# Performance work log

Hardware: AMD Instinct MI355X
Metric: run time of the kernel (lower is better)

## Reference

```python
import jax, jax.numpy as jnp
import numpy as np

B, N, NFEAT = 8, 5000, 15
NUM_CLASSES_IN = 12          # len(elem_labels)
D_IN = NUM_CLASSES_IN + NFEAT - 1  # 26
D_DIST = 256
D_HID = 256
BIN_SIZE = 100
NBINS = N // BIN_SIZE        # 50
K = 16                       # num_neighbors
DIST_MULT = 0.1
MAX_HALF_BINS = 100          # max_num_bins // 2
NUM_ID_OUT, NUM_REG_OUT = 8, 4


def _pairwise_dist(A):
    # A: [nbins, bs, d] -> [nbins, bs, bs]
    na = jnp.sum(A * A, -1)
    d2 = na[..., :, None] - 2.0 * jnp.einsum('...nd,...md->...nm', A, A) + na[..., None, :]
    return jnp.sqrt(jnp.maximum(d2, 1e-6))


def _build_edges(points, rot):
    # points: [N, D_DIST]; LSH binning then per-bin kNN (exp(-dist_mult * dist) affinities)
    mul = points @ rot[:, :NBINS // 2]
    cmul = jnp.concatenate([mul, -mul], axis=-1)
    bin_idx = jnp.argmax(cmul, axis=-1)
    bins_split = jnp.argsort(bin_idx).reshape(NBINS, BIN_SIZE)   # [nbins, bs] point ids
    parts = points[bins_split]                                   # [nbins, bs, d]
    dm = jnp.exp(-DIST_MULT * _pairwise_dist(parts))             # [nbins, bs, bs]
    vals, idx = jax.lax.top_k(dm, K)                             # [nbins, bs, K]
    dst = jax.vmap(lambda b, i: b[i])(bins_split, idx)           # global dst ids
    src = jnp.broadcast_to(bins_split[:, :, None], dst.shape)
    return src.reshape(-1), dst.reshape(-1), vals.reshape(-1)    # nnz = N*K


def _ghconv(x, src, dst, vals, theta, W_h, W_t, b_t):
    # x: [N, H]; edge list (src, dst, vals); duplicates sum, matching tf.sparse.add
    deg = jax.ops.segment_sum(vals, src, num_segments=N)
    norm = jnp.power(deg + 1e-6, -0.5)[:, None]
    f_hom = (x @ theta) * norm
    agg = jax.ops.segment_sum(vals[:, None] * f_hom[dst], src, num_segments=N) * norm
    f_het = x @ W_h
    gate = jax.nn.sigmoid(x @ W_t + b_t)
    return jax.nn.selu(gate * agg + (1.0 - gate) * f_het)


def setup_inputs() -> dict:
    key = jax.random.key(0)
    ks = jax.random.split(key, 32)
    w = lambda i, shape, s=0.02: (s * jax.random.normal(ks[i], shape)).astype(jnp.float32)
    ids = jax.random.randint(ks[0], (B, N, 1), 0, NUM_CLASSES_IN).astype(jnp.float32)
    props = jax.random.normal(ks[1], (B, N, NFEAT - 1), dtype=jnp.float32)
    X = jnp.concatenate([ids, props], axis=-1)
    return {
        'X': X,
        'rot': w(2, (D_DIST, MAX_HALF_BINS), 1.0),
        'W_emb': w(3, (D_IN, D_DIST)), 'b_emb': w(4, (D_DIST,)),
        'Wenc_id': w(5, (D_IN, D_HID)), 'benc_id': w(6, (D_HID,)),
        'theta_id': w(7, (D_HID, D_HID)), 'Wh_id': w(8, (D_HID, D_HID)),
        'Wt_id': w(9, (D_HID, D_HID)), 'bt_id': w(10, (D_HID,)),
        'Wdec_id': w(11, (D_HID, D_HID)), 'bdec_id': w(12, (D_HID,)),
        'Wout_id': w(13, (D_HID, NUM_ID_OUT)), 'bout_id': w(14, (NUM_ID_OUT,)),
        'Wenc_reg': w(15, (D_IN, D_HID)), 'benc_reg': w(16, (D_HID,)),
        'theta_reg': w(17, (D_HID, D_HID)), 'Wh_reg': w(18, (D_HID, D_HID)),
        'Wt_reg': w(19, (D_HID, D_HID)), 'bt_reg': w(20, (D_HID,)),
        'Wdec_reg': w(21, (D_HID, D_HID)), 'bdec_reg': w(22, (D_HID,)),
        'Wout_reg': w(23, (D_HID, NUM_REG_OUT)), 'bout_reg': w(24, (NUM_REG_OUT,)),
    }


def reference(X, rot, W_emb, b_emb,
              Wenc_id, benc_id, theta_id, Wh_id, Wt_id, bt_id, Wdec_id, bdec_id, Wout_id, bout_id,
              Wenc_reg, benc_reg, theta_reg, Wh_reg, Wt_reg, bt_reg, Wdec_reg, bdec_reg, Wout_reg, bout_reg):
    # InputEncoding: one-hot class id + remaining features
    enc = jnp.concatenate(
        [jax.nn.one_hot(X[:, :, 0].astype(jnp.int32), NUM_CLASSES_IN, dtype=jnp.float32),
         X[:, :, 1:]], axis=-1)                                  # [B, N, 26]
    emb = enc @ W_emb + b_emb                                     # distance embedding
    src, dst, vals = jax.vmap(_build_edges, in_axes=(0, None))(emb, rot)

    def branch(Wenc, benc, theta, Wh, Wt, bt, Wdec, bdec, Wout, bout):
        x = jax.nn.selu(enc @ Wenc + benc)
        x = jax.vmap(lambda xb, s, d, v: _ghconv(xb, s, d, v, theta, Wh, Wt, bt))(x, src, dst, vals)
        x = jax.nn.selu(x @ Wdec + bdec)
        return x @ Wout + bout

    out_id = branch(Wenc_id, benc_id, theta_id, Wh_id, Wt_id, bt_id, Wdec_id, bdec_id, Wout_id, bout_id)
    out_reg = branch(Wenc_reg, benc_reg, theta_reg, Wh_reg, Wt_reg, bt_reg, Wdec_reg, bdec_reg, Wout_reg, bout_reg)
    return out_id, out_reg
```

## Files before the change

kernel.cpp:

```cpp
#include <hip/hip_runtime.h>
#include <hip/hip_bf16.h>
#include <cstdint>
#include <cstddef>

#define NB     8
#define NLOC   5000
#define NPTS   40000
#define DIN    26
#define DH     256
#define NBINS  50
#define BSZ    100
#define KNN    16
#define KP     104

static const size_t OFF_BHI  = 40960000;
static const size_t OFF_BLO  = 41353216;
static const size_t OFF_BDHI = 41746432;
static const size_t OFF_BDLO = 41877504;
static const size_t OFF_ENC  = 81920000;
static const size_t OFF_BIN  = 86080000;
static const size_t OFF_ORD  = 86240000;
static const size_t OFF_NRM  = 86400000;
static const size_t OFF_EVAL = 86560000;
static const size_t OFF_EDST = 89120000;
static const size_t OFF_KEYS = 91680000;
static const size_t OFF_AXHI = 91680000;
static const size_t OFF_AXLO = 112160000;
static const size_t OFF_NA   = 132640000;
static const size_t OFF_FHET = 132640000;
static const size_t OFF_GATE = 173600000;

typedef __attribute__((ext_vector_type(8))) short short8;
typedef __attribute__((ext_vector_type(4))) float f32x4;

__device__ __forceinline__ float selu_f(float x) {
  const float scale = 1.0507009873554805f, alpha = 1.6732632423543772f;
  return x > 0.f ? scale * x : scale * alpha * expm1f(x);
}

__device__ __forceinline__ void split_bf16(float v, __hip_bfloat16& h, __hip_bfloat16& l) {
  h = __float2bfloat16(v);
  l = __float2bfloat16(v - __bfloat162float(h));
}

#define EPB 16
__global__ __launch_bounds__(256) void k_enc_emb(
    const float* __restrict__ X, const float* __restrict__ Wemb,
    const float* __restrict__ bemb, float* __restrict__ enc,
    double* __restrict__ emb, double* __restrict__ na_u) {
  __shared__ float xb[EPB * 15];
  __shared__ double partd[EPB][4];
  const int tid = threadIdx.x;
  const int lane = tid & 63, wid = tid >> 6;
  const int r0 = blockIdx.x * EPB;
  if (tid < EPB * 15) xb[tid] = X[(size_t)r0 * 15 + tid];
  double wcol[DIN];
  #pragma unroll
  for (int c = 0; c < DIN; c++) wcol[c] = (double)Wemb[c * DH + tid];
  const double bcol = (double)bemb[tid];
  __syncthreads();
  #pragma unroll 1
  for (int p = 0; p < EPB; p++) {
    const int id = (int)xb[p * 15];
    double acc = 0.0;
    #pragma unroll
    for (int c = 0; c < 12; c++)
      acc += ((c == id) ? 1.0 : 0.0) * wcol[c];
    #pragma unroll
    for (int c = 12; c < DIN; c++)
      acc += (double)xb[p * 15 + (c - 11)] * wcol[c];
    const double v = acc + bcol;
    emb[(size_t)(r0 + p) * DH + tid] = v;
    double sq = v * v;
    #pragma unroll
    for (int off = 32; off >= 1; off >>= 1) sq += __shfl_xor(sq, off);
    if (lane == 0) partd[p][wid] = sq;
  }
  __syncthreads();
  if (tid < EPB)
    na_u[r0 + tid] = partd[tid][0] + partd[tid][1] + partd[tid][2] + partd[tid][3];
  #pragma unroll
  for (int t = 0; t < 2; t++) {
    int idx = t * 256 + tid;
    if (idx < EPB * DIN) {
      int p = idx / DIN, c = idx - p * DIN;
      int id = (int)xb[p * 15];
      float v = (c < 12) ? ((c == id) ? 1.f : 0.f) : xb[p * 15 + (c - 11)];
      enc[(size_t)(r0 + p) * DIN + c] = v;
    }
  }
}

#define MULPTS 16
__global__ __launch_bounds__(512) void k_mul(
    const double* __restrict__ emb, const float* __restrict__ rot,
    int* __restrict__ bin_idx) {
  __shared__ double ebuf[MULPTS][258];
  __shared__ float  rotT[25][257];
  __shared__ double mulb[MULPTS][26];
  const int tid = threadIdx.x;
  const int r0 = blockIdx.x * MULPTS;
  for (int idx = tid; idx < 25 * DH; idx += 512) {
    int d = idx / 25, j = idx - d * 25;
    rotT[j][d] = rot[d * 100 + j];
  }
  for (int idx = tid; idx < MULPTS * DH; idx += 512) {
    int p = idx >> 8, d = idx & 255;
    ebuf[p][d] = emb[(size_t)(r0 + p) * DH + d];
  }
  __syncthreads();
  if (tid < MULPTS * 25) {
    int p = tid / 25, j = tid - p * 25;
    double a = 0.0;
    #pragma unroll 4
    for (int d = 0; d < DH; d++) a += ebuf[p][d] * (double)rotT[j][d];
    mulb[p][j] = a;
  }
  __syncthreads();
  if (tid < MULPTS) {
    double best = -1e300; int bi = 0;
    #pragma unroll 1
    for (int jj = 0; jj < 2 * 25; jj++) {
      double v = (jj < 25) ? mulb[tid][jj] : -mulb[tid][jj - 25];
      if (v > best) { best = v; bi = jj; }
    }
    bin_idx[r0 + tid] = bi;
  }
}

#define SCH 20
__global__ __launch_bounds__(256) void k_sort(
    const int* __restrict__ bin_idx, int* __restrict__ order) {
  const int b = blockIdx.x;
  __shared__ unsigned short cnt[256][NBINS + 2];
  __shared__ int base[NBINS];
  __shared__ int bl[NLOC];
  const int tid = threadIdx.x;
  for (int j = 0; j < NBINS; j++) cnt[tid][j] = 0;
  for (int n = tid; n < NLOC; n += 256) bl[n] = bin_idx[b * NLOC + n];
  __syncthreads();
  const int s = tid * SCH;
  const int e = (s + SCH < NLOC) ? s + SCH : NLOC;
  for (int n = s; n < e; n++) cnt[tid][bl[n]]++;
  __syncthreads();
  if (tid < NBINS) {
    int run = 0;
    for (int t = 0; t < 256; t++) {
      int c = cnt[t][tid];
      cnt[t][tid] = (unsigned short)run;
      run += c;
    }
    base[tid] = run;
  }
  __syncthreads();
  if (tid == 0) {
    int r = 0;
    for (int j = 0; j < NBINS; j++) { int t = base[j]; base[j] = r; r += t; }
  }
  __syncthreads();
  for (int n = s; n < e; n++) {
    int j = bl[n];
    int pos = base[j] + cnt[tid][j];
    cnt[tid][j]++;
    order[b * NLOC + pos] = n;
  }
}

#define DQR 112
__global__ __launch_bounds__(256) void k_dist(
    const double* __restrict__ emb, const int* __restrict__ order,
    const double* __restrict__ na_u, double* __restrict__ keys) {
  __shared__ double P[DQR][34];
  __shared__ double naL[DQR];
  __shared__ int rid[DQR];
  const int bin = blockIdx.x;
  const int rh  = blockIdx.y;
  const int gb0 = bin * BSZ;
  const int brow = (bin / NBINS) * NLOC;
  const int tid = threadIdx.x;
  const int tx = tid & 15, ty = tid >> 4;
  if (tid < DQR) {
    int rr = tid < BSZ ? tid : BSZ - 1;
    int g = brow + order[gb0 + rr];
    rid[tid] = g;
    naL[tid] = na_u[g];
  }
  __syncthreads();
  size_t srow[7];
  int scol[7], sr[7];
  #pragma unroll
  for (int q = 0; q < 7; q++) {
    int idx = q * 256 + tid;
    sr[q] = idx >> 4;
    scol[q] = (idx & 15) * 2;
    srow[q] = (size_t)rid[sr[q]] * DH;
  }
  int ar[4];
  #pragma unroll
  for (int i = 0; i < 4; i++) {
    int pr = rh * 50 + ty + 16 * i;
    ar[i] = pr < DQR ? pr : DQR - 1;
  }
  double acc[4][7] = {};
  double2 buf[7];
  #pragma unroll
  for (int q = 0; q < 7; q++)
    buf[q] = *(const double2*)&emb[srow[q] + scol[q]];
  for (int kc = 0; kc < 8; kc++) {
    __syncthreads();
    #pragma unroll
    for (int q = 0; q < 7; q++) {
      P[sr[q]][scol[q]]     = buf[q].x;
      P[sr[q]][scol[q] + 1] = buf[q].y;
    }
    __syncthreads();
    if (kc < 7) {
      #pragma unroll
      for (int q = 0; q < 7; q++)
        buf[q] = *(const double2*)&emb[srow[q] + (kc + 1) * 32 + scol[q]];
    }
    #pragma unroll 2
    for (int kk = 0; kk < 32; kk++) {
      double b[7];
      #pragma unroll
      for (int j = 0; j < 7; j++) b[j] = P[tx + 16 * j][kk];
      #pragma unroll
      for (int i = 0; i < 4; i++) {
        double a = P[ar[i]][kk];
        #pragma unroll
        for (int j = 0; j < 7; j++) acc[i][j] += a * b[j];
      }
    }
  }
  #pragma unroll
  for (int i = 0; i < 4; i++) {
    int lr = ty + 16 * i;
    if (lr >= 50) continue;
    int gi = rh * 50 + lr;
    #pragma unroll
    for (int j = 0; j < 7; j++) {
      int gj = tx + 16 * j;
      if (gj >= BSZ) continue;
      double t = naL[gi] - 2.0 * acc[i][j];
      t += naL[gj];
      keys[(size_t)(gb0 + gi) * KP + gj] = (t > 1e-6) ? t : 1e-6;
    }
  }
}

__global__ __launch_bounds__(256) void k_topk(
    const double* __restrict__ keys, float* __restrict__ evals,
    int* __restrict__ edstl, float* __restrict__ normv) {
  const int g = threadIdx.x >> 4;
  const int l = threadIdx.x & 15;
  const int row = blockIdx.x * 16 + g;
  const unsigned long long* kr =
      (const unsigned long long*)(keys + (size_t)row * KP);
  unsigned long long c[7];
  #pragma unroll
  for (int s = 0; s < 7; s++) {
    int j = s * 16 + l;
    c[s] = (j < BSZ) ? kr[j] : ~0ull;
  }
  float deg = 0.f, myev = 0.f;
  int myidx = 0;
  #pragma unroll 1
  for (int k = 0; k < KNN; k++) {
    unsigned long long mv = c[0];
    int ms = 0;
    #pragma unroll
    for (int s = 1; s < 7; s++)
      if (c[s] < mv) { mv = c[s]; ms = s; }
    int idx = ms * 16 + l;
    #pragma unroll
    for (int off = 8; off >= 1; off >>= 1) {
      unsigned long long ov = __shfl_xor(mv, off);
      int oi = __shfl_xor(idx, off);
      if (ov < mv || (ov == mv && oi < idx)) { mv = ov; idx = oi; }
    }
    float ev = expf(-0.1f * sqrtf((float)__longlong_as_double(mv)));
    deg += ev;
    if (l == k) { myev = ev; myidx = idx; }
    const int own = idx & 15, slot = idx >> 4;
    if (l == own) {
      #pragma unroll
      for (int s = 0; s < 7; s++)
        if (slot == s) c[s] = ~0ull;
    }
  }
  evals[(size_t)row * KNN + l] = myev;
  edstl[(size_t)row * KNN + l] = myidx;
  if (l == 0) normv[row] = 1.f / sqrtf(deg + 1e-6f);
}

__global__ __launch_bounds__(256) void k_encmm(
    const float* __restrict__ enc, const float* __restrict__ W,
    const float* __restrict__ bias, __hip_bfloat16* __restrict__ hi,
    __hip_bfloat16* __restrict__ lo) {
  const int r = blockIdx.x;
  __shared__ float e[DIN];
  const int tid = threadIdx.x;
  if (tid < DIN) e[tid] = enc[(size_t)r * DIN + tid];
  __syncthreads();
  float acc = 0.f;
  #pragma unroll 1
  for (int c = 0; c < DIN; c++) acc += e[c] * W[c * DH + tid];
  float v = selu_f(acc + bias[tid]);
  __hip_bfloat16 h, l;
  split_bf16(v, h, l);
  hi[(size_t)r * DH + tid] = h;
  lo[(size_t)r * DH + tid] = l;
}

__global__ __launch_bounds__(256) void k_cvt_w4(
    const float* __restrict__ W0, const float* __restrict__ W1,
    const float* __restrict__ W2, const float* __restrict__ W3,
    __hip_bfloat16* __restrict__ Bhi, __hip_bfloat16* __restrict__ Blo,
    __hip_bfloat16* __restrict__ Bdhi, __hip_bfloat16* __restrict__ Bdlo) {
  __shared__ float t[32][33];
  const int z = blockIdx.z;
  const float* W = (z == 0) ? W0 : (z == 1) ? W1 : (z == 2) ? W2 : W3;
  __hip_bfloat16* hi = (z < 3) ? Bhi + (size_t)z * 65536 : Bdhi;
  __hip_bfloat16* lo = (z < 3) ? Blo + (size_t)z * 65536 : Bdlo;
  const int tid = threadIdx.x, tx = tid & 31, ty = tid >> 5;
  const int k0 = blockIdx.x * 32, n0 = blockIdx.y * 32;
  #pragma unroll
  for (int r = 0; r < 4; r++)
    t[ty + r * 8][tx] = W[(size_t)(k0 + ty + r * 8) * 256 + n0 + tx];
  __syncthreads();
  #pragma unroll
  for (int r = 0; r < 4; r++) {
    int n = ty + r * 8;
    float v = t[tx][n];
    __hip_bfloat16 h, l;
    split_bf16(v, h, l);
    hi[(size_t)(n0 + n) * 256 + k0 + tx] = h;
    lo[(size_t)(n0 + n) * 256 + k0 + tx] = l;
  }
}

#define MF_SMEM (4 * 128 * 40 * 2)
template <int MODE>
__global__ __launch_bounds__(256, 4) void k_mfma(
    const ushort* __restrict__ Ahi, const ushort* __restrict__ Alo,
    const ushort* __restrict__ Bhi, const ushort* __restrict__ Blo,
    const float* __restrict__ bias,
    float* __restrict__ O0, float* __restrict__ O1, float* __restrict__ O2) {
  extern __shared__ char mfs[];
  short* As0 = (short*)mfs;
  short* As1 = As0 + 128 * 40;
  short* Bs0 = As1 + 128 * 40;
  short* Bs1 = Bs0 + 128 * 40;
  const int NX = (MODE == 0) ? 6 : 2;
  const int total = NX * 313;
  const int q = total >> 3, rr8 = total & 7;
  const int xcd = blockIdx.x & 7, pos = blockIdx.x >> 3;
  const int lw = (xcd < rr8 ? xcd * (q + 1) : rr8 * (q + 1) + (xcd - rr8) * q) + pos;
  const int m0 = (lw / NX) * 128;
  const int nx = lw - (lw / NX) * NX;
  const int n0 = nx * 128;
  const int tid = threadIdx.x;
  const int lane = tid & 63, wid = tid >> 6;
  const int wr = wid >> 1, wc = wid & 1;
  const int lm = lane & 15, lg = lane >> 4;
  f32x4 acc[4][4];
  #pragma unroll
  for (int i = 0; i < 4; i++)
    #pragma unroll
    for (int j = 0; j < 4; j++)
      #pragma unroll
      for (int r = 0; r < 4; r++) acc[i][j][r] = 0.f;

  for (int k0 = 0; k0 < 256; k0 += 32) {
    #pragma unroll
    for (int it = 0; it < 2; it++) {
      int idx = it * 256 + tid;
      int r = idx >> 2, c = (idx & 3) * 8;
      int gm = m0 + r; if (gm >= NPTS) gm = NPTS - 1;
      *(uint4*)&As0[r * 40 + c] = *(const uint4*)&Ahi[(size_t)gm * 256 + k0 + c];
      *(uint4*)&As1[r * 40 + c] = *(const uint4*)&Alo[(size_t)gm * 256 + k0 + c];
      *(uint4*)&Bs0[r * 40 + c] = *(const uint4*)&Bhi[(size_t)(n0 + r) * 256 + k0 + c];
      *(uint4*)&Bs1[r * 40 + c] = *(const uint4*)&Blo[(size_t)(n0 + r) * 256 + k0 + c];
    }
    __syncthreads();
    const int lk = lg * 8;
    short8 aH[4], bH[4], aL[4], bL[4];
    #pragma unroll
    for (int mf = 0; mf < 4; mf++)
      aH[mf] = *(const short8*)&As0[(wr * 64 + mf * 16 + lm) * 40 + lk];
    #pragma unroll
    for (int nf = 0; nf < 4; nf++)
      bH[nf] = *(const short8*)&Bs0[(wc * 64 + nf * 16 + lm) * 40 + lk];
    #pragma unroll
    for (int mf = 0; mf < 4; mf++)
      #pragma unroll
      for (int nf = 0; nf < 4; nf++)
        acc[mf][nf] = __builtin_amdgcn_mfma_f32_16x16x32_bf16(aH[mf], bH[nf], acc[mf][nf], 0, 0, 0);
    #pragma unroll
    for (int nf = 0; nf < 4; nf++)
      bL[nf] = *(const short8*)&Bs1[(wc * 64 + nf * 16 + lm) * 40 + lk];
    #pragma unroll
    for (int mf = 0; mf < 4; mf++)
      #pragma unroll
      for (int nf = 0; nf < 4; nf++)
        acc[mf][nf] = __builtin_amdgcn_mfma_f32_16x16x32_bf16(aH[mf], bL[nf], acc[mf][nf], 0, 0, 0);
    #pragma unroll
    for (int mf = 0; mf < 4; mf++)
      aL[mf] = *(const short8*)&As1[(wr * 64 + mf * 16 + lm) * 40 + lk];
    #pragma unroll
    for (int mf = 0; mf < 4; mf++)
      #pragma unroll
      for (int nf = 0; nf < 4; nf++)
        acc[mf][nf] = __builtin_amdgcn_mfma_f32_16x16x32_bf16(aL[mf], bH[nf], acc[mf][nf], 0, 0, 0);
    __syncthreads();
  }

  float* Out; int cb;
  if (MODE == 0) {
    const int seg = nx >> 1;
    Out = (seg == 0) ? O0 : ((seg == 1) ? O1 : O2);
    cb = (nx & 1) * 128;
  } else {
    Out = O0; cb = n0;
  }
  const bool do_gate = (MODE == 0) && (nx >> 1) == 2;
  #pragma unroll
  for (int mf = 0; mf < 4; mf++) {
    const int gm0 = m0 + wr * 64 + mf * 16 + lg * 4;
    #pragma unroll
    for (int nf = 0; nf < 4; nf++) {
      const int gn = cb + wc * 64 + nf * 16 + lm;
      #pragma unroll
      for (int r = 0; r < 4; r++) {
        const int gm = gm0 + r;
        if (gm >= NPTS) continue;
        float c = acc[mf][nf][r];
        if (MODE == 1)      c = selu_f(c + bias[gn]);
        else if (do_gate)   c = 1.f / (1.f + expf(-(c + bias[gn])));
        Out[(size_t)gm * 256 + gn] = c;
      }
    }
  }
}

#define GAT_SMEM (100 * 256 * 4 + 1600 * 8 + 100 * 4 + 100 * 4)
__global__ __launch_bounds__(1024) void k_gatherb(
    const float* __restrict__ hth, const float* __restrict__ fhet,
    const float* __restrict__ gate, const float* __restrict__ evals,
    const int* __restrict__ edstl, const int* __restrict__ order,
    const float* __restrict__ normv, __hip_bfloat16* __restrict__ yhi,
    __hip_bfloat16* __restrict__ ylo) {
  extern __shared__ char gsm[];
  float*  hl  = (float*)gsm;
  float2* cwL = (float2*)(gsm + 102400);
  int*    idsL = (int*)(gsm + 102400 + 12800);
  float*  nvL  = (float*)(gsm + 102400 + 12800 + 400);
  const int bin = blockIdx.x;
  const int gb0 = bin * 100;
  const int brow = (bin / NBINS) * NLOC;
  const int tid = threadIdx.x;
  const int p = tid >> 8, d = tid & 255;
  if (tid < BSZ) {
    idsL[tid] = order[gb0 + tid];
    nvL[tid] = normv[gb0 + tid];
  }
  __syncthreads();
  for (int t = tid; t < BSZ * KNN; t += 1024) {
    int lj = edstl[(size_t)gb0 * KNN + t];
    cwL[t] = make_float2(evals[(size_t)gb0 * KNN + t] * nvL[lj],
                         __int_as_float(lj));
  }
  for (int idx = tid; idx < BSZ * DH; idx += 1024) {
    int i = idx >> 8, dd = idx & 255;
    hl[i * 256 + dd] = hth[(size_t)(brow + idsL[i]) * DH + dd];
  }
  __syncthreads();
  size_t srow_n = (size_t)(brow + idsL[p]) * DH;
  float g_n = gate[srow_n + d], fh_n = fhet[srow_n + d];
  #pragma unroll 1
  for (int ii = 0; ii < 25; ii++) {
    const int i = ii * 4 + p;
    const size_t srow = srow_n;
    const float g = g_n, fh = fh_n;
    if (ii < 24) {
      srow_n = (size_t)(brow + idsL[i + 4]) * DH;
      g_n = gate[srow_n + d];
      fh_n = fhet[srow_n + d];
    }
    float acc = 0.f;
    #pragma unroll
    for (int k = 0; k < KNN; k++) {
      float2 cw = cwL[i * KNN + k];
      acc += cw.x * hl[__float_as_int(cw.y) * 256 + d];
    }
    float v = selu_f(g * (nvL[i] * acc) + (1.f - g) * fh);
    __hip_bfloat16 h, l;
    split_bf16(v, h, l);
    yhi[srow + d] = h;
    ylo[srow + d] = l;
  }
}

template <int OW>
__global__ __launch_bounds__(256) void k_out(
    const float* __restrict__ Z, const float* __restrict__ W,
    const float* __restrict__ bias, float* __restrict__ out) {
  const int p0 = blockIdx.x * 32;
  __shared__ float zb[32][257];
  const int tid = threadIdx.x;
  for (int idx = tid; idx < 32 * DH; idx += 256) {
    int p = idx >> 8, d = idx & 255;
    zb[p][d] = Z[(size_t)(p0 + p) * DH + d];
  }
  __syncthreads();
  if (tid < 32 * OW) {
    int p = tid / OW, o = tid - (tid / OW) * OW;
    float acc = 0.f;
    #pragma unroll 4
    for (int d = 0; d < DH; d++) acc += zb[p][d] * W[d * OW + o];
    out[(size_t)(p0 + p) * OW + o] = acc + bias[o];
  }
}

extern "C" void kernel_launch(void* const* d_in, const int* in_sizes, int n_in,
                              void* d_out, int out_size, void* d_ws, size_t ws_size,
                              hipStream_t stream) {
  const float* X     = (const float*)d_in[0];
  const float* rot   = (const float*)d_in[1];
  const float* W_emb = (const float*)d_in[2];
  const float* b_emb = (const float*)d_in[3];
  const float* Wenc[2]  = {(const float*)d_in[4],  (const float*)d_in[14]};
  const float* benc[2]  = {(const float*)d_in[5],  (const float*)d_in[15]};
  const float* theta[2] = {(const float*)d_in[6],  (const float*)d_in[16]};
  const float* Wh[2]    = {(const float*)d_in[7],  (const float*)d_in[17]};
  const float* Wt[2]    = {(const float*)d_in[8],  (const float*)d_in[18]};
  const float* bt[2]    = {(const float*)d_in[9],  (const float*)d_in[19]};
  const float* Wdec[2]  = {(const float*)d_in[10], (const float*)d_in[20]};
  const float* bdec[2]  = {(const float*)d_in[11], (const float*)d_in[21]};
  const float* Wout[2]  = {(const float*)d_in[12], (const float*)d_in[22]};
  const float* bout[2]  = {(const float*)d_in[13], (const float*)d_in[23]};

  char* w = (char*)d_ws;
  double* emb   = (double*)(w + 0);
  float*  hth   = (float*)(w + 0);
  __hip_bfloat16* Bhi  = (__hip_bfloat16*)(w + OFF_BHI);
  __hip_bfloat16* Blo  = (__hip_bfloat16*)(w + OFF_BLO);
  __hip_bfloat16* Bdhi = (__hip_bfloat16*)(w + OFF_BDHI);
  __hip_bfloat16* Bdlo = (__hip_bfloat16*)(w + OFF_BDLO);
  float*  enc   = (float*)(w + OFF_ENC);
  int*    binid = (int*)(w + OFF_BIN);
  int*    order = (int*)(w + OFF_ORD);
  float*  normv = (float*)(w + OFF_NRM);
  float*  evals = (float*)(w + OFF_EVAL);
  int*    edstl = (int*)(w + OFF_EDST);
  double* keys  = (double*)(w + OFF_KEYS);
  double* na_u  = (double*)(w + OFF_NA);
  __hip_bfloat16* Axhi = (__hip_bfloat16*)(w + OFF_AXHI);
  __hip_bfloat16* Axlo = (__hip_bfloat16*)(w + OFF_AXLO);
  float*  fhet  = (float*)(w + OFF_FHET);
  float*  gate  = (float*)(w + OFF_GATE);
  float*  zbuf  = (float*)(w + OFF_GATE);
  float*  outp  = (float*)d_out;

  (void)hipFuncSetAttribute(reinterpret_cast<const void*>(k_gatherb),
                            hipFuncAttributeMaxDynamicSharedMemorySize, GAT_SMEM);
  (void)hipFuncSetAttribute(reinterpret_cast<const void*>(k_mfma<0>),
                            hipFuncAttributeMaxDynamicSharedMemorySize, MF_SMEM);
  (void)hipFuncSetAttribute(reinterpret_cast<const void*>(k_mfma<1>),
                            hipFuncAttributeMaxDynamicSharedMemorySize, MF_SMEM);

  k_enc_emb<<<NPTS / EPB, 256, 0, stream>>>(X, W_emb, b_emb, enc, emb, na_u);
  k_mul<<<NPTS / MULPTS, 512, 0, stream>>>(emb, rot, binid);
  k_sort<<<NB, 256, 0, stream>>>(binid, order);
  k_dist<<<dim3(NB * NBINS, 2), 256, 0, stream>>>(emb, order, na_u, keys);
  k_topk<<<NPTS / 16, 256, 0, stream>>>(keys, evals, edstl, normv);

  const dim3 gw(8, 8, 4);
  for (int br = 0; br < 2; br++) {
    k_cvt_w4<<<gw, 256, 0, stream>>>(theta[br], Wh[br], Wt[br], Wdec[br],
                                     Bhi, Blo, Bdhi, Bdlo);
    k_encmm<<<NPTS, 256, 0, stream>>>(enc, Wenc[br], benc[br], Axhi, Axlo);
    k_mfma<0><<<6 * 313, 256, MF_SMEM, stream>>>((const ushort*)Axhi, (const ushort*)Axlo,
                                                 (const ushort*)Bhi, (const ushort*)Blo,
                                                 bt[br], hth, fhet, gate);
    k_gatherb<<<NB * NBINS, 1024, GAT_SMEM, stream>>>(hth, fhet, gate, evals, edstl,
                                                      order, normv, Axhi, Axlo);
    k_mfma<1><<<2 * 313, 256, MF_SMEM, stream>>>((const ushort*)Axhi, (const ushort*)Axlo,
                                                 (const ushort*)Bdhi, (const ushort*)Bdlo,
                                                 bdec[br], zbuf, nullptr, nullptr);
    if (br == 0) k_out<8><<<NPTS / 32, 256, 0, stream>>>(zbuf, Wout[0], bout[0], outp);
    else         k_out<4><<<NPTS / 32, 256, 0, stream>>>(zbuf, Wout[1], bout[1], outp + (size_t)NPTS * 8);
  }
}
```

Measured before the change: 777.1 us.

## Batch weight conversion, tile encoder matmul, vectorize distance inner loop

The two per-branch weight-conversion launches are merged into one launch writing separate buffers for each branch. The encoder matmul now handles 16 rows per block and keeps its weight column in registers, instead of launching one block per row and rereading W. The distance kernel's inner loop reads shared memory as double2 pairs to halve LDS instructions. The cost is more registers in the encoder and distance kernels and extra workspace for the second branch's weights.

```diff
diff --git a/kernel.cpp b/kernel.cpp
--- a/kernel.cpp
+++ b/kernel.cpp
@@ -13,22 +13,26 @@
 #define KNN    16
 #define KP     104
 
-static const size_t OFF_BHI  = 40960000;
-static const size_t OFF_BLO  = 41353216;
-static const size_t OFF_BDHI = 41746432;
-static const size_t OFF_BDLO = 41877504;
-static const size_t OFF_ENC  = 81920000;
-static const size_t OFF_BIN  = 86080000;
-static const size_t OFF_ORD  = 86240000;
-static const size_t OFF_NRM  = 86400000;
-static const size_t OFF_EVAL = 86560000;
-static const size_t OFF_EDST = 89120000;
-static const size_t OFF_KEYS = 91680000;
-static const size_t OFF_AXHI = 91680000;
-static const size_t OFF_AXLO = 112160000;
-static const size_t OFF_NA   = 132640000;
-static const size_t OFF_FHET = 132640000;
-static const size_t OFF_GATE = 173600000;
+static const size_t OFF_BHI0  = 40960000;
+static const size_t OFF_BLO0  = 41353216;
+static const size_t OFF_BDHI0 = 41746432;
+static const size_t OFF_BDLO0 = 41877504;
+static const size_t OFF_BHI1  = 42100000;
+static const size_t OFF_BLO1  = 42493216;
+static const size_t OFF_BDHI1 = 42886432;
+static const size_t OFF_BDLO1 = 43017504;
+static const size_t OFF_ENC   = 81920000;
+static const size_t OFF_BIN   = 86080000;
+static const size_t OFF_ORD   = 86240000;
+static const size_t OFF_NRM   = 86400000;
+static const size_t OFF_EVAL  = 86560000;
+static const size_t OFF_EDST  = 89120000;
+static const size_t OFF_KEYS  = 91680000;
+static const size_t OFF_AXHI  = 91680000;
+static const size_t OFF_AXLO  = 112160000;
+static const size_t OFF_NA    = 132640000;
+static const size_t OFF_FHET  = 132640000;
+static const size_t OFF_GATE  = 173600000;
 
 typedef __attribute__((ext_vector_type(8))) short short8;
 typedef __attribute__((ext_vector_type(4))) float f32x4;
@@ -219,17 +223,21 @@
       for (int q = 0; q < 7; q++)
         buf[q] = *(const double2*)&emb[srow[q] + (kc + 1) * 32 + scol[q]];
     }
-    #pragma unroll 2
-    for (int kk = 0; kk < 32; kk++) {
-      double b[7];
-      #pragma unroll
-      for (int j = 0; j < 7; j++) b[j] = P[tx + 16 * j][kk];
-      #pragma unroll
-      for (int i = 0; i < 4; i++) {
-        double a = P[ar[i]][kk];
+    #pragma unroll 1
+    for (int kk = 0; kk < 32; kk += 2) {
+      double2 b2[7], a2[4];
+      #pragma unroll
+      for (int j = 0; j < 7; j++) b2[j] = *(const double2*)&P[tx + 16 * j][kk];
+      #pragma unroll
+      for (int i = 0; i < 4; i++) a2[i] = *(const double2*)&P[ar[i]][kk];
+      #pragma unroll
+      for (int i = 0; i < 4; i++)
         #pragma unroll
-        for (int j = 0; j < 7; j++) acc[i][j] += a * b[j];
-      }
+        for (int j = 0; j < 7; j++) acc[i][j] += a2[i].x * b2[j].x;
+      #pragma unroll
+      for (int i = 0; i < 4; i++)
+        #pragma unroll
+        for (int j = 0; j < 7; j++) acc[i][j] += a2[i].y * b2[j].y;
     }
   }
   #pragma unroll
@@ -293,35 +301,52 @@
   if (l == 0) normv[row] = 1.f / sqrtf(deg + 1e-6f);
 }
 
+#define XPB 16
 __global__ __launch_bounds__(256) void k_encmm(
     const float* __restrict__ enc, const float* __restrict__ W,
     const float* __restrict__ bias, __hip_bfloat16* __restrict__ hi,
     __hip_bfloat16* __restrict__ lo) {
-  const int r = blockIdx.x;
-  __shared__ float e[DIN];
-  const int tid = threadIdx.x;
-  if (tid < DIN) e[tid] = enc[(size_t)r * DIN + tid];
-  __syncthreads();
-  float acc = 0.f;
+  __shared__ float eb[XPB * DIN];
+  const int tid = threadIdx.x;
+  const int r0 = blockIdx.x * XPB;
+  for (int idx = tid; idx < XPB * DIN; idx += 256)
+    eb[idx] = enc[(size_t)r0 * DIN + idx];
+  float wcol[DIN];
+  #pragma unroll
+  for (int c = 0; c < DIN; c++) wcol[c] = W[c * DH + tid];
+  const float bcol = bias[tid];
+  __syncthreads();
   #pragma unroll 1
-  for (int c = 0; c < DIN; c++) acc += e[c] * W[c * DH + tid];
-  float v = selu_f(acc + bias[tid]);
-  __hip_bfloat16 h, l;
-  split_bf16(v, h, l);
-  hi[(size_t)r * DH + tid] = h;
-  lo[(size_t)r * DH + tid] = l;
-}
-
-__global__ __launch_bounds__(256) void k_cvt_w4(
+  for (int p = 0; p < XPB; p++) {
+    float acc = 0.f;
+    #pragma unroll
+    for (int c = 0; c < DIN; c++) acc += eb[p * DIN + c] * wcol[c];
+    float v = selu_f(acc + bcol);
+    __hip_bfloat16 h, l;
+    split_bf16(v, h, l);
+    hi[(size_t)(r0 + p) * DH + tid] = h;
+    lo[(size_t)(r0 + p) * DH + tid] = l;
+  }
+}
+
+__global__ __launch_bounds__(256) void k_cvt_w8(
     const float* __restrict__ W0, const float* __restrict__ W1,
     const float* __restrict__ W2, const float* __restrict__ W3,
-    __hip_bfloat16* __restrict__ Bhi, __hip_bfloat16* __restrict__ Blo,
-    __hip_bfloat16* __restrict__ Bdhi, __hip_bfloat16* __restrict__ Bdlo) {
+    const float* __restrict__ W4, const float* __restrict__ W5,
+    const float* __restrict__ W6, const float* __restrict__ W7,
+    __hip_bfloat16* __restrict__ Bhi0, __hip_bfloat16* __restrict__ Blo0,
+    __hip_bfloat16* __restrict__ Bdhi0, __hip_bfloat16* __restrict__ Bdlo0,
+    __hip_bfloat16* __restrict__ Bhi1, __hip_bfloat16* __restrict__ Blo1,
+    __hip_bfloat16* __restrict__ Bdhi1, __hip_bfloat16* __restrict__ Bdlo1) {
   __shared__ float t[32][33];
   const int z = blockIdx.z;
-  const float* W = (z == 0) ? W0 : (z == 1) ? W1 : (z == 2) ? W2 : W3;
-  __hip_bfloat16* hi = (z < 3) ? Bhi + (size_t)z * 65536 : Bdhi;
-  __hip_bfloat16* lo = (z < 3) ? Blo + (size_t)z * 65536 : Bdlo;
+  const float* W = (z == 0) ? W0 : (z == 1) ? W1 : (z == 2) ? W2 : (z == 3) ? W3
+                 : (z == 4) ? W4 : (z == 5) ? W5 : (z == 6) ? W6 : W7;
+  const int zz = z & 3, br = z >> 2;
+  __hip_bfloat16* hi = (zz < 3) ? (br ? Bhi1 : Bhi0) + (size_t)zz * 65536
+                                : (br ? Bdhi1 : Bdhi0);
+  __hip_bfloat16* lo = (zz < 3) ? (br ? Blo1 : Blo0) + (size_t)zz * 65536
+                                : (br ? Bdlo1 : Bdlo0);
   const int tid = threadIdx.x, tx = tid & 31, ty = tid >> 5;
   const int k0 = blockIdx.x * 32, n0 = blockIdx.y * 32;
   #pragma unroll
@@ -543,10 +568,10 @@
   char* w = (char*)d_ws;
   double* emb   = (double*)(w + 0);
   float*  hth   = (float*)(w + 0);
-  __hip_bfloat16* Bhi  = (__hip_bfloat16*)(w + OFF_BHI);
-  __hip_bfloat16* Blo  = (__hip_bfloat16*)(w + OFF_BLO);
-  __hip_bfloat16* Bdhi = (__hip_bfloat16*)(w + OFF_BDHI);
-  __hip_bfloat16* Bdlo = (__hip_bfloat16*)(w + OFF_BDLO);
+  __hip_bfloat16* Bhi[2]  = {(__hip_bfloat16*)(w + OFF_BHI0),  (__hip_bfloat16*)(w + OFF_BHI1)};
+  __hip_bfloat16* Blo[2]  = {(__hip_bfloat16*)(w + OFF_BLO0),  (__hip_bfloat16*)(w + OFF_BLO1)};
+  __hip_bfloat16* Bdhi[2] = {(__hip_bfloat16*)(w + OFF_BDHI0), (__hip_bfloat16*)(w + OFF_BDHI1)};
+  __hip_bfloat16* Bdlo[2] = {(__hip_bfloat16*)(w + OFF_BDLO0), (__hip_bfloat16*)(w + OFF_BDLO1)};
   float*  enc   = (float*)(w + OFF_ENC);
   int*    binid = (int*)(w + OFF_BIN);
   int*    order = (int*)(w + OFF_ORD);
@@ -574,19 +599,19 @@
   k_sort<<<NB, 256, 0, stream>>>(binid, order);
   k_dist<<<dim3(NB * NBINS, 2), 256, 0, stream>>>(emb, order, na_u, keys);
   k_topk<<<NPTS / 16, 256, 0, stream>>>(keys, evals, edstl, normv);
-
-  const dim3 gw(8, 8, 4);
+  k_cvt_w8<<<dim3(8, 8, 8), 256, 0, stream>>>(
+      theta[0], Wh[0], Wt[0], Wdec[0], theta[1], Wh[1], Wt[1], Wdec[1],
+      Bhi[0], Blo[0], Bdhi[0], Bdlo[0], Bhi[1], Blo[1], Bdhi[1], Bdlo[1]);
+
   for (int br = 0; br < 2; br++) {
-    k_cvt_w4<<<gw, 256, 0, stream>>>(theta[br], Wh[br], Wt[br], Wdec[br],
-                                     Bhi, Blo, Bdhi, Bdlo);
-    k_encmm<<<NPTS, 256, 0, stream>>>(enc, Wenc[br], benc[br], Axhi, Axlo);
+    k_encmm<<<NPTS / XPB, 256, 0, stream>>>(enc, Wenc[br], benc[br], Axhi, Axlo);
     k_mfma<0><<<6 * 313, 256, MF_SMEM, stream>>>((const ushort*)Axhi, (const ushort*)Axlo,
-                                                 (const ushort*)Bhi, (const ushort*)Blo,
+                                                 (const ushort*)Bhi[br], (const ushort*)Blo[br],
                                                  bt[br], hth, fhet, gate);
     k_gatherb<<<NB * NBINS, 1024, GAT_SMEM, stream>>>(hth, fhet, gate, evals, edstl,
                                                       order, normv, Axhi, Axlo);
     k_mfma<1><<<2 * 313, 256, MF_SMEM, stream>>>((const ushort*)Axhi, (const ushort*)Axlo,
-                                                 (const ushort*)Bdhi, (const ushort*)Bdlo,
+                                                 (const ushort*)Bdhi[br], (const ushort*)Bdlo[br],
                                                  bdec[br], zbuf, nullptr, nullptr);
     if (br == 0) k_out<8><<<NPTS / 32, 256, 0, stream>>>(zbuf, Wout[0], bout[0], outp);
     else         k_out<4><<<NPTS / 32, 256, 0, stream>>>(zbuf, Wout[1], bout[1], outp + (size_t)NPTS * 8);
```

New measurement: 675.9 us. 13.0% less time.
